# Optimization experiments

Hardware: AMD Instinct MI355X
Metric: run time of the kernel (lower is better)

The kernel has to match this reference:

```python
import jax, jax.numpy as jnp
import numpy as np

N = 100000   # nodes
E = 1600000  # edges (avg degree 16)
D_IN = 128
D_HID = 128
D_OUT = 40
EPS = 1e-5


def _xavier(key, out_f, in_f):
    gain = jnp.sqrt(2.0)  # relu gain, matches nn.init.calculate_gain('relu')
    std = gain * jnp.sqrt(2.0 / (in_f + out_f))
    # uniform xavier bound = sqrt(3)*std
    b = jnp.sqrt(3.0) * std
    return jax.random.uniform(key, (out_f, in_f), jnp.float32, -b, b)


def setup_inputs() -> dict:
    key = jax.random.key(0)
    ks = jax.random.split(key, 10)
    feat = jax.random.normal(ks[0], (N, D_IN), jnp.float32)
    src = jax.random.randint(ks[1], (E,), 0, N, jnp.int32)
    dst = jax.random.randint(ks[2], (E,), 0, N, jnp.int32)
    return {
        "feat": feat,
        "W_self1": _xavier(ks[3], D_HID, D_IN),
        "W_neigh1": _xavier(ks[4], D_HID, D_IN),
        "gamma1": jnp.ones((D_HID,), jnp.float32),
        "beta1": jnp.zeros((D_HID,), jnp.float32),
        "W_self2": _xavier(ks[5], D_HID, D_HID),
        "W_neigh2": _xavier(ks[6], D_HID, D_HID),
        "gamma2": jnp.ones((D_HID,), jnp.float32),
        "beta2": jnp.zeros((D_HID,), jnp.float32),
        "W_self3": _xavier(ks[7], D_OUT, D_HID),
        "W_neigh3": _xavier(ks[8], D_OUT, D_HID),
        "src": src,
        "dst": dst,
    }


def _spmm_mean(x, src, dst):
    # mean aggregation of neighbor features: irregular gather + segment scatter-add
    agg = jax.ops.segment_sum(x[src], dst, num_segments=N)  # [N, d]
    deg = jax.ops.segment_sum(jnp.ones((src.shape[0],), x.dtype), dst, num_segments=N)
    return agg / jnp.maximum(deg, 1.0)[:, None]


def _sage(x, W_self, W_neigh, src, dst):
    return x @ W_self.T + _spmm_mean(x, src, dst) @ W_neigh.T


def _batchnorm(x, gamma, beta):
    mu = jnp.mean(x, axis=0)
    var = jnp.var(x, axis=0)
    return (x - mu) * jax.lax.rsqrt(var + EPS) * gamma + beta


def reference(feat, W_self1, W_neigh1, gamma1, beta1,
              W_self2, W_neigh2, gamma2, beta2,
              W_self3, W_neigh3, src, dst):
    x = _sage(feat, W_self1, W_neigh1, src, dst)
    x = jax.nn.relu(_batchnorm(x, gamma1, beta1))
    x = _sage(x, W_self2, W_neigh2, src, dst)
    x = jax.nn.relu(_batchnorm(x, gamma2, beta2))
    x = _sage(x, W_self3, W_neigh3, src, dst)
    return jax.nn.log_softmax(x, axis=-1)
```

## Files before the change

kernel.cpp:

```cpp
#include <hip/hip_runtime.h>
#include <math.h>

#define NODES 100000
#define EDGES 1600000
#define DH 128
#define DOUT 40

#define BSHIFT 9
#define NBUCK 196
#define HB 200
#define EPB 8000
#define GH (NBUCK * HB)
#define NHS ((GH + 511) / 512)

typedef __attribute__((ext_vector_type(8))) short bf16x8;
typedef __attribute__((ext_vector_type(4))) float f32x4;

__device__ inline ushort bfh(float f) {
    uint u = __float_as_uint(f);
    return (ushort)((u + 0x7FFFu + ((u >> 16) & 1u)) >> 16);
}
__device__ inline float bff(ushort h) { return __uint_as_float(((uint)h) << 16); }


__global__ __launch_bounds__(256) void hist1_kernel(const int* __restrict__ dst,
                                                    uint* __restrict__ ghist) {
    __shared__ uint h[NBUCK];
    int t = threadIdx.x;
    if (t < NBUCK) h[t] = 0;
    __syncthreads();
    int e0 = blockIdx.x * EPB;
    for (int e = e0 + t; e < e0 + EPB; e += 256)
        atomicAdd(&h[((uint)dst[e]) >> BSHIFT], 1u);
    __syncthreads();
    if (t < NBUCK) ghist[t * HB + blockIdx.x] = h[t];
}

__global__ __launch_bounds__(512) void hs1_kernel(const uint* __restrict__ ghist,
                                                  uint* __restrict__ hpart) {
    __shared__ uint buf[512];
    int i = blockIdx.x * 512 + threadIdx.x;
    buf[threadIdx.x] = (i < GH) ? ghist[i] : 0;
    __syncthreads();
    for (int off = 256; off; off >>= 1) {
        if (threadIdx.x < off) buf[threadIdx.x] += buf[threadIdx.x + off];
        __syncthreads();
    }
    if (threadIdx.x == 0) hpart[blockIdx.x] = buf[0];
}

__global__ __launch_bounds__(128) void hs2_kernel(const uint* __restrict__ hpart,
                                                  uint* __restrict__ hpoff,
                                                  int* __restrict__ rowptr,
                                                  int* __restrict__ bucket_base) {
    __shared__ uint buf[128];
    uint v = (threadIdx.x < NHS) ? hpart[threadIdx.x] : 0;
    buf[threadIdx.x] = v;
    __syncthreads();
    for (int off = 1; off < 128; off <<= 1) {
        uint tv = (threadIdx.x >= off) ? buf[threadIdx.x - off] : 0;
        __syncthreads();
        buf[threadIdx.x] += tv;
        __syncthreads();
    }
    if (threadIdx.x < NHS) hpoff[threadIdx.x] = buf[threadIdx.x] - v;
    if (threadIdx.x == 0) { rowptr[NODES] = EDGES; bucket_base[NBUCK] = EDGES; }
}

__global__ __launch_bounds__(512) void hs3_kernel(uint* __restrict__ ghist,
                                                  const uint* __restrict__ hpoff,
                                                  int* __restrict__ bucket_base) {
    __shared__ uint buf[512];
    int i = blockIdx.x * 512 + threadIdx.x;
    uint v = (i < GH) ? ghist[i] : 0;
    buf[threadIdx.x] = v;
    __syncthreads();
    for (int off = 1; off < 512; off <<= 1) {
        uint tv = (threadIdx.x >= off) ? buf[threadIdx.x - off] : 0;
        __syncthreads();
        buf[threadIdx.x] += tv;
        __syncthreads();
    }
    if (i < GH) {
        uint ex = hpoff[blockIdx.x] + buf[threadIdx.x] - v;
        ghist[i] = ex;
        if (i % HB == 0) bucket_base[i / HB] = (int)ex;
    }
}

__global__ __launch_bounds__(256) void scatter1_kernel(const int* __restrict__ src,
                                                       const int* __restrict__ dst,
                                                       const uint* __restrict__ ghist,
                                                       uint2* __restrict__ ebuf) {
    __shared__ uint cur[NBUCK];
    int t = threadIdx.x;
    if (t < NBUCK) cur[t] = ghist[t * HB + blockIdx.x];
    __syncthreads();
    int e0 = blockIdx.x * EPB;
    for (int e = e0 + t; e < e0 + EPB; e += 256) {
        uint d = (uint)dst[e];
        uint s = (uint)src[e];
        uint pos = atomicAdd(&cur[d >> BSHIFT], 1u);
        ebuf[pos] = make_uint2(d, s);
    }
}

__global__ __launch_bounds__(256) void csr2_kernel(const uint2* __restrict__ ebuf,
                                                   const int* __restrict__ bucket_base,
                                                   int* __restrict__ rowptr,
                                                   int* __restrict__ col) {
    __shared__ uint h[512];
    __shared__ uint cur[512];
    __shared__ uint buf[256];
    int b = blockIdx.x;
    int t = threadIdx.x;
    int seg0 = bucket_base[b];
    int seg1 = bucket_base[b + 1];
    h[t] = 0; h[t + 256] = 0;
    __syncthreads();
    uint nbase = (uint)b << BSHIFT;
    for (int e = seg0 + t; e < seg1; e += 256)
        atomicAdd(&h[ebuf[e].x - nbase], 1u);
    __syncthreads();
    uint s0 = h[2 * t], s1 = h[2 * t + 1];
    uint pair = s0 + s1;
    buf[t] = pair;
    __syncthreads();
    for (int off = 1; off < 256; off <<= 1) {
        uint tv = (t >= off) ? buf[t - off] : 0;
        __syncthreads();
        buf[t] += tv;
        __syncthreads();
    }
    uint epre = buf[t] - pair;
    cur[2 * t]     = seg0 + epre;
    cur[2 * t + 1] = seg0 + epre + s0;
    int node0 = (int)nbase + 2 * t;
    if (node0 < NODES)     rowptr[node0]     = seg0 + epre;
    if (node0 + 1 < NODES) rowptr[node0 + 1] = seg0 + epre + s0;
    __syncthreads();
    for (int e = seg0 + t; e < seg1; e += 256) {
        uint2 p = ebuf[e];
        uint pos = atomicAdd(&cur[p.x - nbase], 1u);
        col[pos] = (int)p.y;
    }
}

__global__ void wsplit_all_kernel(const float* __restrict__ Ws1, const float* __restrict__ Wn1,
                                  const float* __restrict__ Ws2, const float* __restrict__ Wn2,
                                  const float* __restrict__ Ws3, const float* __restrict__ Wn3,
                                  ushort* __restrict__ Wh, ushort* __restrict__ Wl) {
    int i = blockIdx.x * blockDim.x + threadIdx.x;
    if (i >= 4 * 16384 + 2 * 6144) return;
    float v;
    if (i < 65536) {
        int which = i >> 14, j = i & 16383;
        const float* W = (which == 0) ? Ws1 : (which == 1) ? Wn1 : (which == 2) ? Ws2 : Wn2;
        v = W[j];
    } else {
        int i2 = i - 65536;
        int which = (i2 >= 6144) ? 1 : 0;
        int j = i2 - which * 6144;
        int n = j >> 7, k = j & 127;
        const float* W = which ? Wn3 : Ws3;
        v = (n < DOUT) ? W[n * 128 + k] : 0.f;
    }
    ushort h = bfh(v);
    Wh[i] = h;
    Wl[i] = bfh(v - bff(h));
}

__global__ void f2b_kernel(const float* __restrict__ f, ushort* __restrict__ b) {
    int i = blockIdx.x * blockDim.x + threadIdx.x;
    float4 v = *reinterpret_cast<const float4*>(f + (size_t)i * 4);
    ushort4 o;
    o.x = bfh(v.x); o.y = bfh(v.y); o.z = bfh(v.z); o.w = bfh(v.w);
    *reinterpret_cast<ushort4*>(b + (size_t)i * 4) = o;
}

__global__ __launch_bounds__(256) void gather_agg_kernel(const ushort* __restrict__ xb,
                                                         const int* __restrict__ rowptr,
                                                         const int* __restrict__ col,
                                                         float* __restrict__ agg) {
    int node = blockIdx.x * 4 + (threadIdx.x >> 6);
    int lane = threadIdx.x & 63;
    int g = lane >> 4;
    int sub = lane & 15;
    int p0 = rowptr[node], p1 = rowptr[node + 1];
    float acc[8] = {};
    for (int p = p0 + g; p < p1; p += 4) {
        int s = col[p];
        uint4 v = *reinterpret_cast<const uint4*>(xb + (size_t)s * 128 + sub * 8);
        acc[0] += bff((ushort)(v.x & 0xffff)); acc[1] += bff((ushort)(v.x >> 16));
        acc[2] += bff((ushort)(v.y & 0xffff)); acc[3] += bff((ushort)(v.y >> 16));
        acc[4] += bff((ushort)(v.z & 0xffff)); acc[5] += bff((ushort)(v.z >> 16));
        acc[6] += bff((ushort)(v.w & 0xffff)); acc[7] += bff((ushort)(v.w >> 16));
    }
#pragma unroll
    for (int j = 0; j < 8; ++j) {
        acc[j] += __shfl_xor(acc[j], 16, 64);
        acc[j] += __shfl_xor(acc[j], 32, 64);
    }
    if (lane < 16) {
        float rd = 1.0f / fmaxf((float)(p1 - p0), 1.0f);
        float4 o0 = make_float4(acc[0] * rd, acc[1] * rd, acc[2] * rd, acc[3] * rd);
        float4 o1 = make_float4(acc[4] * rd, acc[5] * rd, acc[6] * rd, acc[7] * rd);
        *reinterpret_cast<float4*>(agg + (size_t)node * 128 + sub * 8) = o0;
        *reinterpret_cast<float4*>(agg + (size_t)node * 128 + sub * 8 + 4) = o1;
    }
}


__device__ inline void split4(float4 v, ushort4& h, ushort4& l) {
    h.x = bfh(v.x); h.y = bfh(v.y); h.z = bfh(v.z); h.w = bfh(v.w);
    l.x = bfh(v.x - bff(h.x)); l.y = bfh(v.y - bff(h.y));
    l.z = bfh(v.z - bff(h.z)); l.w = bfh(v.w - bff(h.w));
}

#define MFMA(a, b, c) __builtin_amdgcn_mfma_f32_16x16x32_bf16(a, b, c, 0, 0, 0)

__global__ __launch_bounds__(256) void gemm12_kernel(
    const float* __restrict__ x, const float* __restrict__ agg,
    const ushort* __restrict__ Wsh, const ushort* __restrict__ Wsl,
    const ushort* __restrict__ Wnh, const ushort* __restrict__ Wnl,
    float* __restrict__ out, float* __restrict__ stat0) {
    if (blockIdx.x == 0) stat0[threadIdx.x] = 0.f;
    __shared__ ushort xh_s[32 * 128], xl_s[32 * 128], ah_s[32 * 128], al_s[32 * 128];
    int t = threadIdx.x;
    int row0 = blockIdx.x * 32;
#pragma unroll
    for (int i = 0; i < 4; ++i) {
        int c = t + i * 256;
        int r = c >> 5;
        int c0 = (c & 31) * 4;
        int cs = c0 ^ ((r & 7) << 3);
        float4 xv = *reinterpret_cast<const float4*>(x + (size_t)(row0 + r) * 128 + c0);
        float4 av = *reinterpret_cast<const float4*>(agg + (size_t)(row0 + r) * 128 + c0);
        ushort4 h, l;
        split4(xv, h, l);
        *reinterpret_cast<ushort4*>(&xh_s[r * 128 + cs]) = h;
        *reinterpret_cast<ushort4*>(&xl_s[r * 128 + cs]) = l;
        split4(av, h, l);
        *reinterpret_cast<ushort4*>(&ah_s[r * 128 + cs]) = h;
        *reinterpret_cast<ushort4*>(&al_s[r * 128 + cs]) = l;
    }
    __syncthreads();
    int w = t >> 6;
    int l = t & 63;
    int lr = l & 15;
    int kq = (l >> 4) * 8;
    int n0 = w * 32;
    f32x4 acc[2][2] = {};
    for (int kk = 0; kk < 4; ++kk) {
        int kf = kk * 32 + kq;
        bf16x8 a_xh[2], a_xl[2], a_ah[2], a_al[2];
#pragma unroll
        for (int rt = 0; rt < 2; ++rt) {
            int r = rt * 16 + lr;
            int ks = kf ^ ((r & 7) << 3);
            a_xh[rt] = *reinterpret_cast<const bf16x8*>(&xh_s[r * 128 + ks]);
            a_xl[rt] = *reinterpret_cast<const bf16x8*>(&xl_s[r * 128 + ks]);
            a_ah[rt] = *reinterpret_cast<const bf16x8*>(&ah_s[r * 128 + ks]);
            a_al[rt] = *reinterpret_cast<const bf16x8*>(&al_s[r * 128 + ks]);
        }
#pragma unroll
        for (int ct = 0; ct < 2; ++ct) {
            size_t wo = (size_t)(n0 + ct * 16 + lr) * 128 + kf;
            bf16x8 bsh = *reinterpret_cast<const bf16x8*>(Wsh + wo);
            bf16x8 bsl = *reinterpret_cast<const bf16x8*>(Wsl + wo);
            bf16x8 bnh = *reinterpret_cast<const bf16x8*>(Wnh + wo);
            bf16x8 bnl = *reinterpret_cast<const bf16x8*>(Wnl + wo);
#pragma unroll
            for (int rt = 0; rt < 2; ++rt) {
                acc[rt][ct] = MFMA(a_xh[rt], bsh, acc[rt][ct]);
                acc[rt][ct] = MFMA(a_xh[rt], bsl, acc[rt][ct]);
                acc[rt][ct] = MFMA(a_xl[rt], bsh, acc[rt][ct]);
                acc[rt][ct] = MFMA(a_ah[rt], bnh, acc[rt][ct]);
                acc[rt][ct] = MFMA(a_ah[rt], bnl, acc[rt][ct]);
                acc[rt][ct] = MFMA(a_al[rt], bnh, acc[rt][ct]);
            }
        }
    }
    int dr = (l >> 4) * 4;
#pragma unroll
    for (int rt = 0; rt < 2; ++rt)
#pragma unroll
        for (int ct = 0; ct < 2; ++ct)
#pragma unroll
            for (int j = 0; j < 4; ++j)
                out[(size_t)(row0 + rt * 16 + dr + j) * 128 + n0 + ct * 16 + lr] = acc[rt][ct][j];
}

__global__ __launch_bounds__(256) void gemm3_kernel(
    const float* __restrict__ x, const float* __restrict__ agg,
    const ushort* __restrict__ Wsh, const ushort* __restrict__ Wsl,
    const ushort* __restrict__ Wnh, const ushort* __restrict__ Wnl,
    float* __restrict__ out) {
    __shared__ ushort xh_s[64 * 128], xl_s[64 * 128], ah_s[64 * 128], al_s[64 * 128];
    int t = threadIdx.x;
    int row0 = blockIdx.x * 64;
#pragma unroll
    for (int i = 0; i < 8; ++i) {
        int c = t + i * 256;
        int r = c >> 5;
        int c0 = (c & 31) * 4;
        int cs = c0 ^ ((r & 7) << 3);
        int rr = row0 + r; if (rr >= NODES) rr = NODES - 1;
        float4 xv = *reinterpret_cast<const float4*>(x + (size_t)rr * 128 + c0);
        float4 av = *reinterpret_cast<const float4*>(agg + (size_t)rr * 128 + c0);
        ushort4 h, l;
        split4(xv, h, l);
        *reinterpret_cast<ushort4*>(&xh_s[r * 128 + cs]) = h;
        *reinterpret_cast<ushort4*>(&xl_s[r * 128 + cs]) = l;
        split4(av, h, l);
        *reinterpret_cast<ushort4*>(&ah_s[r * 128 + cs]) = h;
        *reinterpret_cast<ushort4*>(&al_s[r * 128 + cs]) = l;
    }
    __syncthreads();
    int w = t >> 6;
    int l = t & 63;
    int lr = l & 15;
    int kq = (l >> 4) * 8;
    f32x4 acc[3] = {};
    for (int kk = 0; kk < 4; ++kk) {
        int kf = kk * 32 + kq;
        int r = w * 16 + lr;
        int ks = kf ^ ((r & 7) << 3);
        bf16x8 a_xh = *reinterpret_cast<const bf16x8*>(&xh_s[r * 128 + ks]);
        bf16x8 a_xl = *reinterpret_cast<const bf16x8*>(&xl_s[r * 128 + ks]);
        bf16x8 a_ah = *reinterpret_cast<const bf16x8*>(&ah_s[r * 128 + ks]);
        bf16x8 a_al = *reinterpret_cast<const bf16x8*>(&al_s[r * 128 + ks]);
#pragma unroll
        for (int ct = 0; ct < 3; ++ct) {
            size_t wo = (size_t)(ct * 16 + lr) * 128 + kf;
            bf16x8 bsh = *reinterpret_cast<const bf16x8*>(Wsh + wo);
            bf16x8 bsl = *reinterpret_cast<const bf16x8*>(Wsl + wo);
            bf16x8 bnh = *reinterpret_cast<const bf16x8*>(Wnh + wo);
            bf16x8 bnl = *reinterpret_cast<const bf16x8*>(Wnl + wo);
            acc[ct] = MFMA(a_xh, bsh, acc[ct]);
            acc[ct] = MFMA(a_xh, bsl, acc[ct]);
            acc[ct] = MFMA(a_xl, bsh, acc[ct]);
            acc[ct] = MFMA(a_ah, bnh, acc[ct]);
            acc[ct] = MFMA(a_ah, bnl, acc[ct]);
            acc[ct] = MFMA(a_al, bnh, acc[ct]);
        }
    }
    int dr = (l >> 4) * 4;
#pragma unroll
    for (int j = 0; j < 4; ++j) {
        float v0 = acc[0][j], v1 = acc[1][j];
        float v2 = (lr < 8) ? acc[2][j] : -INFINITY;
        float m = fmaxf(v0, fmaxf(v1, v2));
#pragma unroll
        for (int o = 8; o; o >>= 1) m = fmaxf(m, __shfl_xor(m, o, 16));
        float e = expf(v0 - m) + expf(v1 - m) + ((lr < 8) ? expf(v2 - m) : 0.f);
#pragma unroll
        for (int o = 8; o; o >>= 1) e += __shfl_xor(e, o, 16);
        float lse = m + logf(e);
        int row = row0 + w * 16 + dr + j;
        if (row < NODES) {
            out[(size_t)row * DOUT + lr] = v0 - lse;
            out[(size_t)row * DOUT + 16 + lr] = v1 - lse;
            if (lr < 8) out[(size_t)row * DOUT + 32 + lr] = acc[2][j] - lse;
        }
    }
}


__global__ __launch_bounds__(256) void bn_stats_kernel(const float* __restrict__ h,
                                                       float* __restrict__ sums,
                                                       float* __restrict__ sumsq) {
    int j = threadIdx.x & 127;
    int half = threadIdx.x >> 7;
    float s = 0.f, q = 0.f;
    for (int i = blockIdx.x * 2 + half; i < NODES; i += gridDim.x * 2) {
        float v = h[(size_t)i * 128 + j];
        s += v; q += v * v;
    }
    __shared__ float ls[256], lq[256];
    ls[threadIdx.x] = s; lq[threadIdx.x] = q;
    __syncthreads();
    if (half == 0) {
        atomicAdd(&sums[j], s + ls[threadIdx.x + 128]);
        atomicAdd(&sumsq[j], q + lq[threadIdx.x + 128]);
    }
}

__global__ void bn_apply_kernel(float* __restrict__ h, ushort* __restrict__ hb,
                                const float* __restrict__ sums, const float* __restrict__ sumsq,
                                const float* __restrict__ gamma, const float* __restrict__ beta) {
    long long t = (long long)blockIdx.x * blockDim.x + threadIdx.x;
    if (t >= (long long)NODES * 32) return;
    int j4 = ((int)(t & 31)) * 4;
    size_t off = (size_t)(t >> 5) * 128 + j4;
    float4 v = *reinterpret_cast<float4*>(h + off);
    float4 s4 = *reinterpret_cast<const float4*>(sums + j4);
    float4 q4 = *reinterpret_cast<const float4*>(sumsq + j4);
    float4 g4 = *reinterpret_cast<const float4*>(gamma + j4);
    float4 be4 = *reinterpret_cast<const float4*>(beta + j4);
    const float inv = 1.0f / NODES;
    float m, var, a;
    m = s4.x * inv; var = q4.x * inv - m * m; a = g4.x * rsqrtf(var + 1e-5f);
    v.x = fmaxf(v.x * a + (be4.x - m * a), 0.f);
    m = s4.y * inv; var = q4.y * inv - m * m; a = g4.y * rsqrtf(var + 1e-5f);
    v.y = fmaxf(v.y * a + (be4.y - m * a), 0.f);
    m = s4.z * inv; var = q4.z * inv - m * m; a = g4.z * rsqrtf(var + 1e-5f);
    v.z = fmaxf(v.z * a + (be4.z - m * a), 0.f);
    m = s4.w * inv; var = q4.w * inv - m * m; a = g4.w * rsqrtf(var + 1e-5f);
    v.w = fmaxf(v.w * a + (be4.w - m * a), 0.f);
    *reinterpret_cast<float4*>(h + off) = v;
    ushort4 o;
    o.x = bfh(v.x); o.y = bfh(v.y); o.z = bfh(v.z); o.w = bfh(v.w);
    *reinterpret_cast<ushort4*>(hb + off) = o;
}

extern "C" void kernel_launch(void* const* d_in, const int* in_sizes, int n_in,
                              void* d_out, int out_size, void* d_ws, size_t ws_size,
                              hipStream_t stream) {
    const float* feat   = (const float*)d_in[0];
    const float* Ws1    = (const float*)d_in[1];
    const float* Wn1    = (const float*)d_in[2];
    const float* gamma1 = (const float*)d_in[3];
    const float* beta1  = (const float*)d_in[4];
    const float* Ws2    = (const float*)d_in[5];
    const float* Wn2    = (const float*)d_in[6];
    const float* gamma2 = (const float*)d_in[7];
    const float* beta2  = (const float*)d_in[8];
    const float* Ws3    = (const float*)d_in[9];
    const float* Wn3    = (const float*)d_in[10];
    const int*   src    = (const int*)d_in[11];
    const int*   dst    = (const int*)d_in[12];
    float* out = (float*)d_out;

    float* ws = (float*)d_ws;
    const size_t NF = (size_t)NODES * 128;
    float* xbuf = ws;
    float* agg  = ws + NF;
    float* sums  = ws + 2 * NF;
    float* sumsq = sums + 128;
    ushort* xb   = (ushort*)(sumsq + 128);
    ushort* Wh   = xb + NF;
    ushort* Wl   = Wh + 77824;
    int* rowptr = (int*)(Wl + 77824);
    uint* ghist = (uint*)(rowptr + NODES + 1);
    uint* hpart = ghist + GH;
    uint* hpoff = hpart + 128;
    int* bucket_base = (int*)(hpoff + 128);
    int* col    = bucket_base + NBUCK + 1;
    uint2* ebuf = (uint2*)agg;

    ushort* Wsh1 = Wh;           ushort* Wsl1 = Wl;
    ushort* Wnh1 = Wh + 16384;   ushort* Wnl1 = Wl + 16384;
    ushort* Wsh2 = Wh + 32768;   ushort* Wsl2 = Wl + 32768;
    ushort* Wnh2 = Wh + 49152;   ushort* Wnl2 = Wl + 49152;
    ushort* Wsh3 = Wh + 65536;   ushort* Wsl3 = Wl + 65536;
    ushort* Wnh3 = Wh + 71680;   ushort* Wnl3 = Wl + 71680;

    const int GEMM_GRID  = NODES / 32;
    const int GEMM3_GRID = (NODES + 63) / 64;
    const int AGG_GRID   = NODES / 4;

    hist1_kernel<<<HB, 256, 0, stream>>>(dst, ghist);
    hs1_kernel<<<NHS, 512, 0, stream>>>(ghist, hpart);
    hs2_kernel<<<1, 128, 0, stream>>>(hpart, hpoff, rowptr, bucket_base);
    hs3_kernel<<<NHS, 512, 0, stream>>>(ghist, hpoff, bucket_base);
    scatter1_kernel<<<HB, 256, 0, stream>>>(src, dst, ghist, ebuf);
    csr2_kernel<<<NBUCK, 256, 0, stream>>>(ebuf, bucket_base, rowptr, col);

    wsplit_all_kernel<<<304, 256, 0, stream>>>(Ws1, Wn1, Ws2, Wn2, Ws3, Wn3, Wh, Wl);
    f2b_kernel<<<(int)(NF / 4 / 256), 256, 0, stream>>>(feat, xb);

    gather_agg_kernel<<<AGG_GRID, 256, 0, stream>>>(xb, rowptr, col, agg);
    gemm12_kernel<<<GEMM_GRID, 256, 0, stream>>>(feat, agg, Wsh1, Wsl1, Wnh1, Wnl1, xbuf, sums);
    bn_stats_kernel<<<1024, 256, 0, stream>>>(xbuf, sums, sumsq);
    bn_apply_kernel<<<(NODES * 32) / 256, 256, 0, stream>>>(xbuf, xb, sums, sumsq, gamma1, beta1);

    gather_agg_kernel<<<AGG_GRID, 256, 0, stream>>>(xb, rowptr, col, agg);
    gemm12_kernel<<<GEMM_GRID, 256, 0, stream>>>(xbuf, agg, Wsh2, Wsl2, Wnh2, Wnl2, xbuf, sums);
    bn_stats_kernel<<<1024, 256, 0, stream>>>(xbuf, sums, sumsq);
    bn_apply_kernel<<<(NODES * 32) / 256, 256, 0, stream>>>(xbuf, xb, sums, sumsq, gamma2, beta2);

    gather_agg_kernel<<<AGG_GRID, 256, 0, stream>>>(xb, rowptr, col, agg);
    gemm3_kernel<<<GEMM3_GRID, 256, 0, stream>>>(xbuf, agg, Wsh3, Wsl3, Wnh3, Wnl3, out);
}
```

Before: 678.8 us.

## Fuse neighbor aggregation into SAGE GEMMs and compute BN partials in-epilogue

Each layer now gathers and averages neighbor bf16 features inside the GEMM kernel, split into hi/lo straight into shared memory, so the fp32 agg buffer is neither written nor read back. Features are stored pre-split as hi/lo bf16 arrays, so GEMM prologues copy them instead of converting fp32. BatchNorm sums and sums of squares are reduced per block in the GEMM epilogue, and a small reduction kernel replaces the full-pass stats kernel. The fused kernels have fewer waves per node for the gather (8 or 16 rows per wave, serialized), which may lower latency hiding for the irregular loads.

```diff
diff --git a/kernel.cpp b/kernel.cpp
--- a/kernel.cpp
+++ b/kernel.cpp
@@ -170,83 +170,80 @@
     Wl[i] = bfh(v - bff(h));
 }
 
-__global__ void f2b_kernel(const float* __restrict__ f, ushort* __restrict__ b) {
+__global__ void fsplit_kernel(const float* __restrict__ f, ushort* __restrict__ xh,
+                              ushort* __restrict__ xl) {
     int i = blockIdx.x * blockDim.x + threadIdx.x;
     float4 v = *reinterpret_cast<const float4*>(f + (size_t)i * 4);
-    ushort4 o;
-    o.x = bfh(v.x); o.y = bfh(v.y); o.z = bfh(v.z); o.w = bfh(v.w);
-    *reinterpret_cast<ushort4*>(b + (size_t)i * 4) = o;
-}
-
-__global__ __launch_bounds__(256) void gather_agg_kernel(const ushort* __restrict__ xb,
-                                                         const int* __restrict__ rowptr,
-                                                         const int* __restrict__ col,
-                                                         float* __restrict__ agg) {
-    int node = blockIdx.x * 4 + (threadIdx.x >> 6);
-    int lane = threadIdx.x & 63;
-    int g = lane >> 4;
-    int sub = lane & 15;
-    int p0 = rowptr[node], p1 = rowptr[node + 1];
-    float acc[8] = {};
-    for (int p = p0 + g; p < p1; p += 4) {
-        int s = col[p];
-        uint4 v = *reinterpret_cast<const uint4*>(xb + (size_t)s * 128 + sub * 8);
-        acc[0] += bff((ushort)(v.x & 0xffff)); acc[1] += bff((ushort)(v.x >> 16));
-        acc[2] += bff((ushort)(v.y & 0xffff)); acc[3] += bff((ushort)(v.y >> 16));
-        acc[4] += bff((ushort)(v.z & 0xffff)); acc[5] += bff((ushort)(v.z >> 16));
-        acc[6] += bff((ushort)(v.w & 0xffff)); acc[7] += bff((ushort)(v.w >> 16));
-    }
-#pragma unroll
-    for (int j = 0; j < 8; ++j) {
-        acc[j] += __shfl_xor(acc[j], 16, 64);
-        acc[j] += __shfl_xor(acc[j], 32, 64);
-    }
-    if (lane < 16) {
-        float rd = 1.0f / fmaxf((float)(p1 - p0), 1.0f);
-        float4 o0 = make_float4(acc[0] * rd, acc[1] * rd, acc[2] * rd, acc[3] * rd);
-        float4 o1 = make_float4(acc[4] * rd, acc[5] * rd, acc[6] * rd, acc[7] * rd);
-        *reinterpret_cast<float4*>(agg + (size_t)node * 128 + sub * 8) = o0;
-        *reinterpret_cast<float4*>(agg + (size_t)node * 128 + sub * 8 + 4) = o1;
-    }
-}
-
-
-__device__ inline void split4(float4 v, ushort4& h, ushort4& l) {
+    ushort4 h, l;
     h.x = bfh(v.x); h.y = bfh(v.y); h.z = bfh(v.z); h.w = bfh(v.w);
     l.x = bfh(v.x - bff(h.x)); l.y = bfh(v.y - bff(h.y));
     l.z = bfh(v.z - bff(h.z)); l.w = bfh(v.w - bff(h.w));
+    *reinterpret_cast<ushort4*>(xh + (size_t)i * 4) = h;
+    *reinterpret_cast<ushort4*>(xl + (size_t)i * 4) = l;
 }
 
 #define MFMA(a, b, c) __builtin_amdgcn_mfma_f32_16x16x32_bf16(a, b, c, 0, 0, 0)
 
-__global__ __launch_bounds__(256) void gemm12_kernel(
-    const float* __restrict__ x, const float* __restrict__ agg,
+__global__ __launch_bounds__(256) void gemm12_fused(
+    const ushort* __restrict__ xh, const ushort* __restrict__ xl,
+    const int* __restrict__ rowptr, const int* __restrict__ col,
     const ushort* __restrict__ Wsh, const ushort* __restrict__ Wsl,
     const ushort* __restrict__ Wnh, const ushort* __restrict__ Wnl,
-    float* __restrict__ out, float* __restrict__ stat0) {
+    float* __restrict__ out, float* __restrict__ partials, float* __restrict__ stat0) {
     if (blockIdx.x == 0) stat0[threadIdx.x] = 0.f;
     __shared__ ushort xh_s[32 * 128], xl_s[32 * 128], ah_s[32 * 128], al_s[32 * 128];
     int t = threadIdx.x;
     int row0 = blockIdx.x * 32;
 #pragma unroll
-    for (int i = 0; i < 4; ++i) {
-        int c = t + i * 256;
-        int r = c >> 5;
-        int c0 = (c & 31) * 4;
+    for (int i = 0; i < 2; ++i) {
+        int f = t + i * 256;
+        int r = f >> 4;
+        int c0 = (f & 15) * 8;
         int cs = c0 ^ ((r & 7) << 3);
-        float4 xv = *reinterpret_cast<const float4*>(x + (size_t)(row0 + r) * 128 + c0);
-        float4 av = *reinterpret_cast<const float4*>(agg + (size_t)(row0 + r) * 128 + c0);
-        ushort4 h, l;
-        split4(xv, h, l);
-        *reinterpret_cast<ushort4*>(&xh_s[r * 128 + cs]) = h;
-        *reinterpret_cast<ushort4*>(&xl_s[r * 128 + cs]) = l;
-        split4(av, h, l);
-        *reinterpret_cast<ushort4*>(&ah_s[r * 128 + cs]) = h;
-        *reinterpret_cast<ushort4*>(&al_s[r * 128 + cs]) = l;
-    }
-    __syncthreads();
+        *reinterpret_cast<uint4*>(&xh_s[r * 128 + cs]) =
+            *reinterpret_cast<const uint4*>(xh + (size_t)(row0 + r) * 128 + c0);
+        *reinterpret_cast<uint4*>(&xl_s[r * 128 + cs]) =
+            *reinterpret_cast<const uint4*>(xl + (size_t)(row0 + r) * 128 + c0);
+    }
     int w = t >> 6;
     int l = t & 63;
+    int g = l >> 4;
+    int sub = l & 15;
+#pragma unroll
+    for (int i = 0; i < 8; ++i) {
+        int r = w * 8 + i;
+        int node = row0 + r;
+        int p0 = rowptr[node], p1 = rowptr[node + 1];
+        float acc[8] = {};
+        for (int p = p0 + g; p < p1; p += 4) {
+            int s = col[p];
+            uint4 v = *reinterpret_cast<const uint4*>(xh + (size_t)s * 128 + sub * 8);
+            acc[0] += bff((ushort)(v.x & 0xffff)); acc[1] += bff((ushort)(v.x >> 16));
+            acc[2] += bff((ushort)(v.y & 0xffff)); acc[3] += bff((ushort)(v.y >> 16));
+            acc[4] += bff((ushort)(v.z & 0xffff)); acc[5] += bff((ushort)(v.z >> 16));
+            acc[6] += bff((ushort)(v.w & 0xffff)); acc[7] += bff((ushort)(v.w >> 16));
+        }
+#pragma unroll
+        for (int j = 0; j < 8; ++j) {
+            acc[j] += __shfl_xor(acc[j], 16, 64);
+            acc[j] += __shfl_xor(acc[j], 32, 64);
+        }
+        if (l < 16) {
+            float rd = 1.0f / fmaxf((float)(p1 - p0), 1.0f);
+            bf16x8 hi, lo;
+#pragma unroll
+            for (int j = 0; j < 8; ++j) {
+                float m = acc[j] * rd;
+                ushort hb = bfh(m);
+                hi[j] = (short)hb;
+                lo[j] = (short)bfh(m - bff(hb));
+            }
+            int cs = (sub * 8) ^ ((r & 7) << 3);
+            *reinterpret_cast<bf16x8*>(&ah_s[r * 128 + cs]) = hi;
+            *reinterpret_cast<bf16x8*>(&al_s[r * 128 + cs]) = lo;
+        }
+    }
+    __syncthreads();
     int lr = l & 15;
     int kq = (l >> 4) * 8;
     int n0 = w * 32;
@@ -289,10 +286,69 @@
 #pragma unroll
             for (int j = 0; j < 4; ++j)
                 out[(size_t)(row0 + rt * 16 + dr + j) * 128 + n0 + ct * 16 + lr] = acc[rt][ct][j];
-}
-
-__global__ __launch_bounds__(256) void gemm3_kernel(
-    const float* __restrict__ x, const float* __restrict__ agg,
+    float s0 = 0.f, q0 = 0.f, s1 = 0.f, q1 = 0.f;
+#pragma unroll
+    for (int rt = 0; rt < 2; ++rt)
+#pragma unroll
+        for (int j = 0; j < 4; ++j) {
+            float v0 = acc[rt][0][j], v1 = acc[rt][1][j];
+            s0 += v0; q0 += v0 * v0;
+            s1 += v1; q1 += v1 * v1;
+        }
+    s0 += __shfl_xor(s0, 16, 64); s0 += __shfl_xor(s0, 32, 64);
+    q0 += __shfl_xor(q0, 16, 64); q0 += __shfl_xor(q0, 32, 64);
+    s1 += __shfl_xor(s1, 16, 64); s1 += __shfl_xor(s1, 32, 64);
+    q1 += __shfl_xor(q1, 16, 64); q1 += __shfl_xor(q1, 32, 64);
+    if (l < 16) {
+        float* pb = partials + (size_t)blockIdx.x * 256;
+        pb[n0 + lr] = s0;
+        pb[n0 + 16 + lr] = s1;
+        pb[128 + n0 + lr] = q0;
+        pb[128 + n0 + 16 + lr] = q1;
+    }
+}
+
+__global__ __launch_bounds__(256) void bnred_kernel(const float* __restrict__ partials,
+                                                    float* __restrict__ stats, int nblk) {
+    float s = 0.f;
+    for (int b = blockIdx.x; b < nblk; b += gridDim.x)
+        s += partials[(size_t)b * 256 + threadIdx.x];
+    atomicAdd(&stats[threadIdx.x], s);
+}
+
+__global__ void bn_apply_kernel(const float* __restrict__ h, ushort* __restrict__ xh,
+                                ushort* __restrict__ xl, const float* __restrict__ stats,
+                                const float* __restrict__ gamma, const float* __restrict__ beta) {
+    long long t = (long long)blockIdx.x * blockDim.x + threadIdx.x;
+    if (t >= (long long)NODES * 32) return;
+    int j4 = ((int)(t & 31)) * 4;
+    size_t off = (size_t)(t >> 5) * 128 + j4;
+    float4 v = *reinterpret_cast<const float4*>(h + off);
+    float4 s4 = *reinterpret_cast<const float4*>(stats + j4);
+    float4 q4 = *reinterpret_cast<const float4*>(stats + 128 + j4);
+    float4 g4 = *reinterpret_cast<const float4*>(gamma + j4);
+    float4 be4 = *reinterpret_cast<const float4*>(beta + j4);
+    const float inv = 1.0f / NODES;
+    float m, var, a;
+    m = s4.x * inv; var = q4.x * inv - m * m; a = g4.x * rsqrtf(var + 1e-5f);
+    v.x = fmaxf(v.x * a + (be4.x - m * a), 0.f);
+    m = s4.y * inv; var = q4.y * inv - m * m; a = g4.y * rsqrtf(var + 1e-5f);
+    v.y = fmaxf(v.y * a + (be4.y - m * a), 0.f);
+    m = s4.z * inv; var = q4.z * inv - m * m; a = g4.z * rsqrtf(var + 1e-5f);
+    v.z = fmaxf(v.z * a + (be4.z - m * a), 0.f);
+    m = s4.w * inv; var = q4.w * inv - m * m; a = g4.w * rsqrtf(var + 1e-5f);
+    v.w = fmaxf(v.w * a + (be4.w - m * a), 0.f);
+    ushort4 hh, ll;
+    hh.x = bfh(v.x); hh.y = bfh(v.y); hh.z = bfh(v.z); hh.w = bfh(v.w);
+    ll.x = bfh(v.x - bff(hh.x)); ll.y = bfh(v.y - bff(hh.y));
+    ll.z = bfh(v.z - bff(hh.z)); ll.w = bfh(v.w - bff(hh.w));
+    *reinterpret_cast<ushort4*>(xh + off) = hh;
+    *reinterpret_cast<ushort4*>(xl + off) = ll;
+}
+
+__global__ __launch_bounds__(256) void gemm3_fused(
+    const ushort* __restrict__ xh, const ushort* __restrict__ xl,
+    const int* __restrict__ rowptr, const int* __restrict__ col,
     const ushort* __restrict__ Wsh, const ushort* __restrict__ Wsl,
     const ushort* __restrict__ Wnh, const ushort* __restrict__ Wnl,
     float* __restrict__ out) {
@@ -300,25 +356,56 @@
     int t = threadIdx.x;
     int row0 = blockIdx.x * 64;
 #pragma unroll
-    for (int i = 0; i < 8; ++i) {
-        int c = t + i * 256;
-        int r = c >> 5;
-        int c0 = (c & 31) * 4;
+    for (int i = 0; i < 4; ++i) {
+        int f = t + i * 256;
+        int r = f >> 4;
+        int c0 = (f & 15) * 8;
         int cs = c0 ^ ((r & 7) << 3);
         int rr = row0 + r; if (rr >= NODES) rr = NODES - 1;
-        float4 xv = *reinterpret_cast<const float4*>(x + (size_t)rr * 128 + c0);
-        float4 av = *reinterpret_cast<const float4*>(agg + (size_t)rr * 128 + c0);
-        ushort4 h, l;
-        split4(xv, h, l);
-        *reinterpret_cast<ushort4*>(&xh_s[r * 128 + cs]) = h;
-        *reinterpret_cast<ushort4*>(&xl_s[r * 128 + cs]) = l;
-        split4(av, h, l);
-        *reinterpret_cast<ushort4*>(&ah_s[r * 128 + cs]) = h;
-        *reinterpret_cast<ushort4*>(&al_s[r * 128 + cs]) = l;
-    }
-    __syncthreads();
+        *reinterpret_cast<uint4*>(&xh_s[r * 128 + cs]) =
+            *reinterpret_cast<const uint4*>(xh + (size_t)rr * 128 + c0);
+        *reinterpret_cast<uint4*>(&xl_s[r * 128 + cs]) =
+            *reinterpret_cast<const uint4*>(xl + (size_t)rr * 128 + c0);
+    }
     int w = t >> 6;
     int l = t & 63;
+    int g = l >> 4;
+    int sub = l & 15;
+#pragma unroll
+    for (int i = 0; i < 16; ++i) {
+        int r = w * 16 + i;
+        int node = row0 + r; if (node >= NODES) node = NODES - 1;
+        int p0 = rowptr[node], p1 = rowptr[node + 1];
+        float acc[8] = {};
+        for (int p = p0 + g; p < p1; p += 4) {
+            int s = col[p];
+            uint4 v = *reinterpret_cast<const uint4*>(xh + (size_t)s * 128 + sub * 8);
+            acc[0] += bff((ushort)(v.x & 0xffff)); acc[1] += bff((ushort)(v.x >> 16));
+            acc[2] += bff((ushort)(v.y & 0xffff)); acc[3] += bff((ushort)(v.y >> 16));
+            acc[4] += bff((ushort)(v.z & 0xffff)); acc[5] += bff((ushort)(v.z >> 16));
+            acc[6] += bff((ushort)(v.w & 0xffff)); acc[7] += bff((ushort)(v.w >> 16));
+        }
+#pragma unroll
+        for (int j = 0; j < 8; ++j) {
+            acc[j] += __shfl_xor(acc[j], 16, 64);
+            acc[j] += __shfl_xor(acc[j], 32, 64);
+        }
+        if (l < 16) {
+            float rd = 1.0f / fmaxf((float)(p1 - p0), 1.0f);
+            bf16x8 hi, lo;
+#pragma unroll
+            for (int j = 0; j < 8; ++j) {
+                float m = acc[j] * rd;
+                ushort hb = bfh(m);
+                hi[j] = (short)hb;
+                lo[j] = (short)bfh(m - bff(hb));
+            }
+            int cs = (sub * 8) ^ ((r & 7) << 3);
+            *reinterpret_cast<bf16x8*>(&ah_s[r * 128 + cs]) = hi;
+            *reinterpret_cast<bf16x8*>(&al_s[r * 128 + cs]) = lo;
+        }
+    }
+    __syncthreads();
     int lr = l & 15;
     int kq = (l >> 4) * 8;
     f32x4 acc[3] = {};
@@ -364,54 +451,6 @@
             if (lr < 8) out[(size_t)row * DOUT + 32 + lr] = acc[2][j] - lse;
         }
     }
-}
-
-
-__global__ __launch_bounds__(256) void bn_stats_kernel(const float* __restrict__ h,
-                                                       float* __restrict__ sums,
-                                                       float* __restrict__ sumsq) {
-    int j = threadIdx.x & 127;
-    int half = threadIdx.x >> 7;
-    float s = 0.f, q = 0.f;
-    for (int i = blockIdx.x * 2 + half; i < NODES; i += gridDim.x * 2) {
-        float v = h[(size_t)i * 128 + j];
-        s += v; q += v * v;
-    }
-    __shared__ float ls[256], lq[256];
-    ls[threadIdx.x] = s; lq[threadIdx.x] = q;
-    __syncthreads();
-    if (half == 0) {
-        atomicAdd(&sums[j], s + ls[threadIdx.x + 128]);
-        atomicAdd(&sumsq[j], q + lq[threadIdx.x + 128]);
-    }
-}
-
-__global__ void bn_apply_kernel(float* __restrict__ h, ushort* __restrict__ hb,
-                                const float* __restrict__ sums, const float* __restrict__ sumsq,
-                                const float* __restrict__ gamma, const float* __restrict__ beta) {
-    long long t = (long long)blockIdx.x * blockDim.x + threadIdx.x;
-    if (t >= (long long)NODES * 32) return;
-    int j4 = ((int)(t & 31)) * 4;
-    size_t off = (size_t)(t >> 5) * 128 + j4;
-    float4 v = *reinterpret_cast<float4*>(h + off);
-    float4 s4 = *reinterpret_cast<const float4*>(sums + j4);
-    float4 q4 = *reinterpret_cast<const float4*>(sumsq + j4);
-    float4 g4 = *reinterpret_cast<const float4*>(gamma + j4);
-    float4 be4 = *reinterpret_cast<const float4*>(beta + j4);
-    const float inv = 1.0f / NODES;
-    float m, var, a;
-    m = s4.x * inv; var = q4.x * inv - m * m; a = g4.x * rsqrtf(var + 1e-5f);
-    v.x = fmaxf(v.x * a + (be4.x - m * a), 0.f);
-    m = s4.y * inv; var = q4.y * inv - m * m; a = g4.y * rsqrtf(var + 1e-5f);
-    v.y = fmaxf(v.y * a + (be4.y - m * a), 0.f);
-    m = s4.z * inv; var = q4.z * inv - m * m; a = g4.z * rsqrtf(var + 1e-5f);
-    v.z = fmaxf(v.z * a + (be4.z - m * a), 0.f);
-    m = s4.w * inv; var = q4.w * inv - m * m; a = g4.w * rsqrtf(var + 1e-5f);
-    v.w = fmaxf(v.w * a + (be4.w - m * a), 0.f);
-    *reinterpret_cast<float4*>(h + off) = v;
-    ushort4 o;
-    o.x = bfh(v.x); o.y = bfh(v.y); o.z = bfh(v.z); o.w = bfh(v.w);
-    *reinterpret_cast<ushort4*>(hb + off) = o;
 }
 
 extern "C" void kernel_launch(void* const* d_in, const int* in_sizes, int n_in,
@@ -435,19 +474,19 @@
     float* ws = (float*)d_ws;
     const size_t NF = (size_t)NODES * 128;
     float* xbuf = ws;
-    float* agg  = ws + NF;
-    float* sums  = ws + 2 * NF;
-    float* sumsq = sums + 128;
-    ushort* xb   = (ushort*)(sumsq + 128);
-    ushort* Wh   = xb + NF;
-    ushort* Wl   = Wh + 77824;
+    float* stats = ws + NF;
+    float* partials = stats + 256;
+    ushort* xh = (ushort*)(partials + 3125 * 256);
+    ushort* xl = xh + NF;
+    ushort* Wh = xl + NF;
+    ushort* Wl = Wh + 77824;
     int* rowptr = (int*)(Wl + 77824);
     uint* ghist = (uint*)(rowptr + NODES + 1);
     uint* hpart = ghist + GH;
     uint* hpoff = hpart + 128;
     int* bucket_base = (int*)(hpoff + 128);
     int* col    = bucket_base + NBUCK + 1;
-    uint2* ebuf = (uint2*)agg;
+    uint2* ebuf = (uint2*)xbuf;
 
     ushort* Wsh1 = Wh;           ushort* Wsl1 = Wl;
     ushort* Wnh1 = Wh + 16384;   ushort* Wnl1 = Wl + 16384;
@@ -458,7 +497,6 @@
 
     const int GEMM_GRID  = NODES / 32;
     const int GEMM3_GRID = (NODES + 63) / 64;
-    const int AGG_GRID   = NODES / 4;
 
     hist1_kernel<<<HB, 256, 0, stream>>>(dst, ghist);
     hs1_kernel<<<NHS, 512, 0, stream>>>(ghist, hpart);
@@ -468,18 +506,18 @@
     csr2_kernel<<<NBUCK, 256, 0, stream>>>(ebuf, bucket_base, rowptr, col);
 
     wsplit_all_kernel<<<304, 256, 0, stream>>>(Ws1, Wn1, Ws2, Wn2, Ws3, Wn3, Wh, Wl);
-    f2b_kernel<<<(int)(NF / 4 / 256), 256, 0, stream>>>(feat, xb);
-
-    gather_agg_kernel<<<AGG_GRID, 256, 0, stream>>>(xb, rowptr, col, agg);
-    gemm12_kernel<<<GEMM_GRID, 256, 0, stream>>>(feat, agg, Wsh1, Wsl1, Wnh1, Wnl1, xbuf, sums);
-    bn_stats_kernel<<<1024, 256, 0, stream>>>(xbuf, sums, sumsq);
-    bn_apply_kernel<<<(NODES * 32) / 256, 256, 0, stream>>>(xbuf, xb, sums, sumsq, gamma1, beta1);
-
-    gather_agg_kernel<<<AGG_GRID, 256, 0, stream>>>(xb, rowptr, col, agg);
-    gemm12_kernel<<<GEMM_GRID, 256, 0, stream>>>(xbuf, agg, Wsh2, Wsl2, Wnh2, Wnl2, xbuf, sums);
-    bn_stats_kernel<<<1024, 256, 0, stream>>>(xbuf, sums, sumsq);
-    bn_apply_kernel<<<(NODES * 32) / 256, 256, 0, stream>>>(xbuf, xb, sums, sumsq, gamma2, beta2);
-
-    gather_agg_kernel<<<AGG_GRID, 256, 0, stream>>>(xb, rowptr, col, agg);
-    gemm3_kernel<<<GEMM3_GRID, 256, 0, stream>>>(xbuf, agg, Wsh3, Wsl3, Wnh3, Wnl3, out);
-}
+    fsplit_kernel<<<(int)(NF / 4 / 256), 256, 0, stream>>>(feat, xh, xl);
+
+    gemm12_fused<<<GEMM_GRID, 256, 0, stream>>>(xh, xl, rowptr, col,
+                                                Wsh1, Wsl1, Wnh1, Wnl1, xbuf, partials, stats);
+    bnred_kernel<<<64, 256, 0, stream>>>(partials, stats, GEMM_GRID);
+    bn_apply_kernel<<<(NODES * 32) / 256, 256, 0, stream>>>(xbuf, xh, xl, stats, gamma1, beta1);
+
+    gemm12_fused<<<GEMM_GRID, 256, 0, stream>>>(xh, xl, rowptr, col,
+                                                Wsh2, Wsl2, Wnh2, Wnl2, xbuf, partials, stats);
+    bnred_kernel<<<64, 256, 0, stream>>>(partials, stats, GEMM_GRID);
+    bn_apply_kernel<<<(NODES * 32) / 256, 256, 0, stream>>>(xbuf, xh, xl, stats, gamma2, beta2);
+
+    gemm3_fused<<<GEMM3_GRID, 256, 0, stream>>>(xh, xl, rowptr, col,
+                                                Wsh3, Wsl3, Wnh3, Wnl3, out);
+}
```

Measured after the change: 794.9 us. +17.1%, slower.
